# Optimization experiments

Hardware: AMD Instinct MI355X
Metric: run time of the kernel (lower is better)

Reference implementation:

```python
import jax, jax.numpy as jnp
import numpy as np

B, C, N, HID = 1, 64, 1024, 128


def setup_inputs() -> dict:
    key = jax.random.key(0)
    k1, k2, k3, k4, k5 = jax.random.split(key, 5)
    x = jax.random.normal(k1, (B, C, N), dtype=jnp.float32)
    # Conv2d(2C -> HID, 1): weight [HID, 2C] (1x1 kernel flattened), bias [HID]
    W1 = jax.random.normal(k2, (HID, 2 * C), dtype=jnp.float32) * (1.0 / np.sqrt(2 * C))
    b1 = jax.random.normal(k3, (HID,), dtype=jnp.float32) * 0.01
    # Conv2d(HID -> 1, 1): weight [HID], bias [1]
    W2 = jax.random.normal(k4, (HID,), dtype=jnp.float32) * (1.0 / np.sqrt(HID))
    b2 = jax.random.normal(k5, (1,), dtype=jnp.float32) * 0.01
    return {"x": x, "W1": W1, "b1": b1, "W2": W2, "b2": b2}


def reference(x, W1, b1, W2, b2):
    # Original: m1[b,c,i,j] = x[b,c,j]; m2[b,c,i,j] = x[b,c,i]; block = cat([m1, m2], dim=1)
    # tanh is elementwise, and the 1x1 conv is linear, so we split W1 into the
    # halves acting on m1 (j-indexed) and m2 (i-indexed) and avoid the explicit
    # O(N^2 * 2C) repeat+concat. The nonlinear hidden tensor [B,HID,N,N] is the
    # same math as Conv2d(tanh(block)).
    c = x.shape[1]
    t = jnp.tanh(x)                                   # [B, C, N]
    pj = jnp.einsum('hc,bcn->bhn', W1[:, :c], t)      # contribution of m1 (varies over j)
    pi = jnp.einsum('hc,bcn->bhn', W1[:, c:], t)      # contribution of m2 (varies over i)
    h = jnp.tanh(pi[:, :, :, None] + pj[:, :, None, :] + b1[None, :, None, None])  # [B,HID,N,N]
    e = jnp.einsum('h,bhij->bij', W2, h) + b2[0]      # [B, N, N]
    return e + jnp.swapaxes(e, 1, 2)
```

## Files before the change

kernel.cpp:

```cpp
#include <hip/hip_runtime.h>
#include <math.h>

#define CN   64
#define NN   1024
#define HIDN 128
#define NDIAG 528
#define NOFF  496

__device__ __forceinline__ float tanh_fast(float x) {
    float e = __expf(2.0f * x);
    return 1.0f - 2.0f * __builtin_amdgcn_rcpf(e + 1.0f);
}

__global__ __launch_bounds__(256) void prep_kernel(
    const float* __restrict__ x, const float* __restrict__ W1,
    const float* __restrict__ b1, float2* __restrict__ S)
{
    __shared__ float t_s[2][64];
    const int tid = threadIdx.x;
    const int n0  = blockIdx.x * 2;

    if (tid < 64) {
        float2 xv = *(const float2*)&x[tid * NN + n0];
        t_s[0][tid] = tanh_fast(xv.x);
        t_s[1][tid] = tanh_fast(xv.y);
    }
    __syncthreads();

    const int h  = tid & 127;
    const int nl = tid >> 7;
    const float4* wrow = (const float4*)(W1 + h * (2 * CN));

    float pj[4] = {0.f, 0.f, 0.f, 0.f};
    float pi[4] = {0.f, 0.f, 0.f, 0.f};
#pragma unroll
    for (int c4 = 0; c4 < 16; ++c4) {
        float4 tv = *(const float4*)&t_s[nl][c4 * 4];
        float4 wl = wrow[c4];
        float4 wh = wrow[16 + c4];
        const int s = c4 & 3;
        pj[s] = fmaf(wl.x, tv.x, fmaf(wl.y, tv.y, fmaf(wl.z, tv.z, fmaf(wl.w, tv.w, pj[s]))));
        pi[s] = fmaf(wh.x, tv.x, fmaf(wh.y, tv.y, fmaf(wh.z, tv.z, fmaf(wh.w, tv.w, pi[s]))));
    }
    float pjs = (pj[0] + pj[1]) + (pj[2] + pj[3]);
    float pis = (pi[0] + pi[1]) + (pi[2] + pi[3]);
    float U = tanh_fast(pis + b1[h]);
    float V = tanh_fast(pjs);
    S[h * NN + n0 + nl] = make_float2(U, V);
}

__device__ __forceinline__ void sym_term(float w2h, float2 A, float2 B, float& acc)
{
    float d1 = fmaf(A.x, B.y, 1.0f);
    float d2 = fmaf(B.x, A.y, 1.0f);
    float n1 = A.x + B.y;
    float n2 = B.x + A.y;
    float r  = __builtin_amdgcn_rcpf(d1 * d2);
    float t  = fmaf(n1, d2, n2 * d1);
    acc = fmaf(w2h, t * r, acc);
}

__global__ __launch_bounds__(256) void pair_kernel(
    const float2* __restrict__ S, const float* __restrict__ W2,
    const float* __restrict__ b2, float* __restrict__ out)
{
    const int id = blockIdx.x;
    int bi, bj, h0, nchunk;
    bool chunk1;
    if (id < NDIAG) {
        int t = id;
        int r = (int)((sqrtf(8.f * t + 1.f) - 1.f) * 0.5f);
        while ((r + 1) * (r + 2) / 2 <= t) ++r;
        while (r * (r + 1) / 2 > t) --r;
        int c = t - r * (r + 1) / 2;
        bi = c; bj = r; chunk1 = false;
        h0 = 0; nchunk = (bi == bj) ? 4 : 2;
    } else {
        int t = id - NDIAG;
        int r = (int)((1.f + sqrtf(8.f * t + 1.f)) * 0.5f);
        while (r * (r - 1) / 2 > t) --r;
        while (r * (r + 1) / 2 <= t) ++r;
        int c = t - r * (r - 1) / 2;
        bi = c; bj = r; chunk1 = true;
        h0 = 64; nchunk = 2;
    }

    __shared__ float2 Si[32][32];
    __shared__ float2 Sj[32][32];

    const int tid = threadIdx.x;
    const int tx = tid & 15, ty = tid >> 4;
    const int i0 = bi * 32, j0 = bj * 32;

    float acc00 = 0.f, acc01 = 0.f, acc10 = 0.f, acc11 = 0.f;

    for (int hc = 0; hc < nchunk; ++hc) {
        const int hbase = h0 + hc * 32;
        __syncthreads();
#pragma unroll
        for (int k = 0; k < 4; ++k) {
            int t2 = tid + k * 256;
            int hl = t2 >> 5, nl = t2 & 31;
            Si[hl][nl] = S[(hbase + hl) * NN + i0 + nl];
            Sj[hl][nl] = S[(hbase + hl) * NN + j0 + nl];
        }
        __syncthreads();
#pragma unroll 8
        for (int hl = 0; hl < 32; ++hl) {
            float w2h = W2[hbase + hl];
            float2 A0 = Si[hl][ty];
            float2 A1 = Si[hl][ty + 16];
            float2 B0 = Sj[hl][tx];
            float2 B1 = Sj[hl][tx + 16];
            sym_term(w2h, A0, B0, acc00);
            sym_term(w2h, A0, B1, acc01);
            sym_term(w2h, A1, B0, acc10);
            sym_term(w2h, A1, B1, acc11);
        }
    }

    if (!chunk1) {
        float v00 = acc00, v01 = acc01, v10 = acc10, v11 = acc11;
        if (bi == bj) {
            const float bias2 = 2.0f * b2[0];
            v00 += bias2; v01 += bias2; v10 += bias2; v11 += bias2;
        }
        out[(i0 + ty)      * NN + j0 + tx]      = v00;
        out[(i0 + ty)      * NN + j0 + tx + 16] = v01;
        out[(i0 + ty + 16) * NN + j0 + tx]      = v10;
        out[(i0 + ty + 16) * NN + j0 + tx + 16] = v11;
    } else {
        __syncthreads();
        float* T = (float*)&Si[0][0];
        T[ty * 33 + tx]             = acc00;
        T[ty * 33 + tx + 16]        = acc01;
        T[(ty + 16) * 33 + tx]      = acc10;
        T[(ty + 16) * 33 + tx + 16] = acc11;
        __syncthreads();
        out[(j0 + ty)      * NN + i0 + tx]      = T[tx * 33 + ty];
        out[(j0 + ty)      * NN + i0 + tx + 16] = T[(tx + 16) * 33 + ty];
        out[(j0 + ty + 16) * NN + i0 + tx]      = T[tx * 33 + ty + 16];
        out[(j0 + ty + 16) * NN + i0 + tx + 16] = T[(tx + 16) * 33 + ty + 16];
    }
}

__global__ __launch_bounds__(256) void combine_kernel(
    const float* __restrict__ b2, float* __restrict__ out)
{
    int t = blockIdx.x;
    int r = (int)((1.f + sqrtf(8.f * t + 1.f)) * 0.5f);
    while (r * (r - 1) / 2 > t) --r;
    while (r * (r + 1) / 2 <= t) ++r;
    int c = t - r * (r - 1) / 2;
    const int i0 = c * 32, j0 = r * 32;

    __shared__ float Ua[32][33];
    __shared__ float Lb[32][33];
    const int tid = threadIdx.x;
    const int tx = tid & 15, ty = tid >> 4;

    Ua[ty][tx]           = out[(i0 + ty)      * NN + j0 + tx];
    Ua[ty][tx + 16]      = out[(i0 + ty)      * NN + j0 + tx + 16];
    Ua[ty + 16][tx]      = out[(i0 + ty + 16) * NN + j0 + tx];
    Ua[ty + 16][tx + 16] = out[(i0 + ty + 16) * NN + j0 + tx + 16];
    Lb[ty][tx]           = out[(j0 + ty)      * NN + i0 + tx];
    Lb[ty][tx + 16]      = out[(j0 + ty)      * NN + i0 + tx + 16];
    Lb[ty + 16][tx]      = out[(j0 + ty + 16) * NN + i0 + tx];
    Lb[ty + 16][tx + 16] = out[(j0 + ty + 16) * NN + i0 + tx + 16];
    __syncthreads();

    const float bias2 = 2.0f * b2[0];
#pragma unroll
    for (int k = 0; k < 4; ++k) {
        int ry = ty + (k >> 1) * 16;
        int cx = tx + (k & 1) * 16;
        out[(i0 + ry) * NN + j0 + cx] = Ua[ry][cx] + Lb[cx][ry] + bias2;
    }
#pragma unroll
    for (int k = 0; k < 4; ++k) {
        int ry = ty + (k >> 1) * 16;
        int cx = tx + (k & 1) * 16;
        out[(j0 + ry) * NN + i0 + cx] = Ua[cx][ry] + Lb[ry][cx] + bias2;
    }
}

extern "C" void kernel_launch(void* const* d_in, const int* in_sizes, int n_in,
                              void* d_out, int out_size, void* d_ws, size_t ws_size,
                              hipStream_t stream)
{
    const float* x  = (const float*)d_in[0];
    const float* W1 = (const float*)d_in[1];
    const float* b1 = (const float*)d_in[2];
    const float* W2 = (const float*)d_in[3];
    const float* b2 = (const float*)d_in[4];
    float* out = (float*)d_out;
    float2* S  = (float2*)d_ws;

    prep_kernel<<<512, 256, 0, stream>>>(x, W1, b1, S);
    pair_kernel<<<NDIAG + NOFF, 256, 0, stream>>>(S, W2, b2, out);
    combine_kernel<<<NOFF, 256, 0, stream>>>(b2, out);
}
```

Before: 98.91 us.

## Split hidden dim into 8 chunks with 4x4 register tiles and workspace reduction

The pair kernel now launches 8 single-wavefront blocks per upper-triangular tile pair, each covering 16 hidden units with a 4x4 per-thread register tile. Per-row and per-column terms are precomputed so the inner loop needs fewer operations per pair. Partial sums go to a workspace that the combine kernel reduces, adding the bias and writing both the tile and its transpose. This is meant to raise parallelism and per-thread reuse, at the cost of extra workspace traffic (about 17 MB of partials written and read back).

```diff
diff --git a/kernel.cpp b/kernel.cpp
--- a/kernel.cpp
+++ b/kernel.cpp
@@ -1,11 +1,10 @@
 #include <hip/hip_runtime.h>
 #include <math.h>
 
-#define CN   64
-#define NN   1024
-#define HIDN 128
-#define NDIAG 528
-#define NOFF  496
+#define CN    64
+#define NN    1024
+#define NPAIR 528
+#define NCHUNK 8
 
 __device__ __forceinline__ float tanh_fast(float x) {
     float e = __expf(2.0f * x);
@@ -49,138 +48,124 @@
     S[h * NN + n0 + nl] = make_float2(U, V);
 }
 
-__device__ __forceinline__ void sym_term(float w2h, float2 A, float2 B, float& acc)
-{
-    float d1 = fmaf(A.x, B.y, 1.0f);
-    float d2 = fmaf(B.x, A.y, 1.0f);
-    float n1 = A.x + B.y;
-    float n2 = B.x + A.y;
-    float r  = __builtin_amdgcn_rcpf(d1 * d2);
-    float t  = fmaf(n1, d2, n2 * d1);
-    acc = fmaf(w2h, t * r, acc);
-}
-
-__global__ __launch_bounds__(256) void pair_kernel(
+__global__ __launch_bounds__(64) void pair_kernel(
     const float2* __restrict__ S, const float* __restrict__ W2,
-    const float* __restrict__ b2, float* __restrict__ out)
+    float* __restrict__ ws)
 {
     const int id = blockIdx.x;
-    int bi, bj, h0, nchunk;
-    bool chunk1;
-    if (id < NDIAG) {
-        int t = id;
-        int r = (int)((sqrtf(8.f * t + 1.f) - 1.f) * 0.5f);
-        while ((r + 1) * (r + 2) / 2 <= t) ++r;
-        while (r * (r + 1) / 2 > t) --r;
-        int c = t - r * (r + 1) / 2;
-        bi = c; bj = r; chunk1 = false;
-        h0 = 0; nchunk = (bi == bj) ? 4 : 2;
-    } else {
-        int t = id - NDIAG;
-        int r = (int)((1.f + sqrtf(8.f * t + 1.f)) * 0.5f);
-        while (r * (r - 1) / 2 > t) --r;
-        while (r * (r + 1) / 2 <= t) ++r;
-        int c = t - r * (r - 1) / 2;
-        bi = c; bj = r; chunk1 = true;
-        h0 = 64; nchunk = 2;
+    const int pair = id >> 3, chunk = id & 7;
+    int r = (int)((sqrtf(8.f * pair + 1.f) - 1.f) * 0.5f);
+    while ((r + 1) * (r + 2) / 2 <= pair) ++r;
+    while (r * (r + 1) / 2 > pair) --r;
+    const int bi = pair - r * (r + 1) / 2, bj = r;
+    const int i0 = bi * 32, j0 = bj * 32, h0 = chunk * 16;
+
+    __shared__ float2 Si[16 * 32];
+    __shared__ float2 Sj[16 * 32];
+    const int lane = threadIdx.x;
+
+    {
+        float4* SiF = (float4*)Si;
+        float4* SjF = (float4*)Sj;
+        const float4* SF = (const float4*)S;
+#pragma unroll
+        for (int k = 0; k < 4; ++k) {
+            int t = k * 64 + lane;
+            int row = t >> 4, seg = t & 15;
+            SiF[t] = SF[(((h0 + row) * NN + i0) >> 1) + seg];
+            SjF[t] = SF[(((h0 + row) * NN + j0) >> 1) + seg];
+        }
+    }
+    __syncthreads();
+
+    const int la = lane & 7, lb = lane >> 3;
+    float acc[4][4];
+#pragma unroll
+    for (int m = 0; m < 4; ++m)
+#pragma unroll
+        for (int n = 0; n < 4; ++n) acc[m][n] = 0.f;
+
+#pragma unroll 4
+    for (int h = 0; h < 16; ++h) {
+        const float w2h = W2[h0 + h];
+        float2 A[4], B[4];
+#pragma unroll
+        for (int m = 0; m < 4; ++m) A[m] = Si[h * 32 + la + 8 * m];
+#pragma unroll
+        for (int n = 0; n < 4; ++n) B[n] = Sj[h * 32 + lb + 8 * n];
+        float PA[4], QA[4], PB[4], QB[4];
+#pragma unroll
+        for (int m = 0; m < 4; ++m) {
+            PA[m] = w2h * (A[m].x + A[m].y);
+            QA[m] = fmaf(A[m].x, A[m].y, 1.0f);
+        }
+#pragma unroll
+        for (int n = 0; n < 4; ++n) {
+            PB[n] = w2h * (B[n].x + B[n].y);
+            QB[n] = fmaf(B[n].x, B[n].y, 1.0f);
+        }
+#pragma unroll
+        for (int m = 0; m < 4; ++m)
+#pragma unroll
+            for (int n = 0; n < 4; ++n) {
+                float d1 = fmaf(A[m].x, B[n].y, 1.0f);
+                float d2 = fmaf(B[n].x, A[m].y, 1.0f);
+                float rr = __builtin_amdgcn_rcpf(d1 * d2);
+                float Np = fmaf(PA[m], QB[n], PB[n] * QA[m]);
+                acc[m][n] = fmaf(Np, rr, acc[m][n]);
+            }
     }
 
-    __shared__ float2 Si[32][32];
-    __shared__ float2 Sj[32][32];
-
-    const int tid = threadIdx.x;
-    const int tx = tid & 15, ty = tid >> 4;
-    const int i0 = bi * 32, j0 = bj * 32;
-
-    float acc00 = 0.f, acc01 = 0.f, acc10 = 0.f, acc11 = 0.f;
-
-    for (int hc = 0; hc < nchunk; ++hc) {
-        const int hbase = h0 + hc * 32;
-        __syncthreads();
+    float* wsp = ws + (pair * NCHUNK + chunk) * 1024;
 #pragma unroll
-        for (int k = 0; k < 4; ++k) {
-            int t2 = tid + k * 256;
-            int hl = t2 >> 5, nl = t2 & 31;
-            Si[hl][nl] = S[(hbase + hl) * NN + i0 + nl];
-            Sj[hl][nl] = S[(hbase + hl) * NN + j0 + nl];
-        }
-        __syncthreads();
-#pragma unroll 8
-        for (int hl = 0; hl < 32; ++hl) {
-            float w2h = W2[hbase + hl];
-            float2 A0 = Si[hl][ty];
-            float2 A1 = Si[hl][ty + 16];
-            float2 B0 = Sj[hl][tx];
-            float2 B1 = Sj[hl][tx + 16];
-            sym_term(w2h, A0, B0, acc00);
-            sym_term(w2h, A0, B1, acc01);
-            sym_term(w2h, A1, B0, acc10);
-            sym_term(w2h, A1, B1, acc11);
-        }
-    }
-
-    if (!chunk1) {
-        float v00 = acc00, v01 = acc01, v10 = acc10, v11 = acc11;
-        if (bi == bj) {
-            const float bias2 = 2.0f * b2[0];
-            v00 += bias2; v01 += bias2; v10 += bias2; v11 += bias2;
-        }
-        out[(i0 + ty)      * NN + j0 + tx]      = v00;
-        out[(i0 + ty)      * NN + j0 + tx + 16] = v01;
-        out[(i0 + ty + 16) * NN + j0 + tx]      = v10;
-        out[(i0 + ty + 16) * NN + j0 + tx + 16] = v11;
-    } else {
-        __syncthreads();
-        float* T = (float*)&Si[0][0];
-        T[ty * 33 + tx]             = acc00;
-        T[ty * 33 + tx + 16]        = acc01;
-        T[(ty + 16) * 33 + tx]      = acc10;
-        T[(ty + 16) * 33 + tx + 16] = acc11;
-        __syncthreads();
-        out[(j0 + ty)      * NN + i0 + tx]      = T[tx * 33 + ty];
-        out[(j0 + ty)      * NN + i0 + tx + 16] = T[(tx + 16) * 33 + ty];
-        out[(j0 + ty + 16) * NN + i0 + tx]      = T[tx * 33 + ty + 16];
-        out[(j0 + ty + 16) * NN + i0 + tx + 16] = T[(tx + 16) * 33 + ty + 16];
-    }
+    for (int m = 0; m < 4; ++m)
+#pragma unroll
+        for (int n = 0; n < 4; ++n)
+            wsp[(m * 4 + n) * 64 + lane] = acc[m][n];
 }
 
 __global__ __launch_bounds__(256) void combine_kernel(
-    const float* __restrict__ b2, float* __restrict__ out)
+    const float* __restrict__ ws, const float* __restrict__ b2,
+    float* __restrict__ out)
 {
-    int t = blockIdx.x;
-    int r = (int)((1.f + sqrtf(8.f * t + 1.f)) * 0.5f);
-    while (r * (r - 1) / 2 > t) --r;
-    while (r * (r + 1) / 2 <= t) ++r;
-    int c = t - r * (r - 1) / 2;
-    const int i0 = c * 32, j0 = r * 32;
+    const int pair = blockIdx.x;
+    int r = (int)((sqrtf(8.f * pair + 1.f) - 1.f) * 0.5f);
+    while ((r + 1) * (r + 2) / 2 <= pair) ++r;
+    while (r * (r + 1) / 2 > pair) --r;
+    const int bi = pair - r * (r + 1) / 2, bj = r;
+    const int i0 = bi * 32, j0 = bj * 32;
 
-    __shared__ float Ua[32][33];
-    __shared__ float Lb[32][33];
-    const int tid = threadIdx.x;
-    const int tx = tid & 15, ty = tid >> 4;
+    __shared__ float T[32 * 35];
+    const int t = threadIdx.x;
+    const int lane_p = t & 63, q0 = t >> 6;
+    const int la = lane_p & 7, lb = (lane_p >> 3) & 7;
+    const float bias2 = 2.0f * b2[0];
+    const float* wsp = ws + pair * NCHUNK * 1024;
 
-    Ua[ty][tx]           = out[(i0 + ty)      * NN + j0 + tx];
-    Ua[ty][tx + 16]      = out[(i0 + ty)      * NN + j0 + tx + 16];
-    Ua[ty + 16][tx]      = out[(i0 + ty + 16) * NN + j0 + tx];
-    Ua[ty + 16][tx + 16] = out[(i0 + ty + 16) * NN + j0 + tx + 16];
-    Lb[ty][tx]           = out[(j0 + ty)      * NN + i0 + tx];
-    Lb[ty][tx + 16]      = out[(j0 + ty)      * NN + i0 + tx + 16];
-    Lb[ty + 16][tx]      = out[(j0 + ty + 16) * NN + i0 + tx];
-    Lb[ty + 16][tx + 16] = out[(j0 + ty + 16) * NN + i0 + tx + 16];
+#pragma unroll
+    for (int k = 0; k < 4; ++k) {
+        float a = 0.f;
+#pragma unroll
+        for (int cc = 0; cc < NCHUNK; ++cc)
+            a += wsp[cc * 1024 + (q0 + 4 * k) * 64 + lane_p];
+        T[(la + 8 * k) * 35 + lb + 8 * q0] = a + bias2;
+    }
     __syncthreads();
 
-    const float bias2 = 2.0f * b2[0];
+    const int tx = t & 15, ty = t >> 4;
 #pragma unroll
     for (int k = 0; k < 4; ++k) {
-        int ry = ty + (k >> 1) * 16;
-        int cx = tx + (k & 1) * 16;
-        out[(i0 + ry) * NN + j0 + cx] = Ua[ry][cx] + Lb[cx][ry] + bias2;
+        int rr2 = ty + (k >> 1) * 16;
+        int cc2 = tx + (k & 1) * 16;
+        out[(i0 + rr2) * NN + j0 + cc2] = T[rr2 * 35 + cc2];
     }
+    if (bi != bj) {
 #pragma unroll
-    for (int k = 0; k < 4; ++k) {
-        int ry = ty + (k >> 1) * 16;
-        int cx = tx + (k & 1) * 16;
-        out[(j0 + ry) * NN + i0 + cx] = Ua[cx][ry] + Lb[ry][cx] + bias2;
+        for (int k = 0; k < 4; ++k) {
+            int rr2 = ty + (k >> 1) * 16;
+            int cc2 = tx + (k & 1) * 16;
+            out[(j0 + rr2) * NN + i0 + cc2] = T[cc2 * 35 + rr2];
+        }
     }
 }
 
@@ -194,9 +179,11 @@
     const float* W2 = (const float*)d_in[3];
     const float* b2 = (const float*)d_in[4];
     float* out = (float*)d_out;
-    float2* S  = (float2*)d_ws;
+
+    float2* S   = (float2*)d_ws;
+    float*  par = (float*)((char*)d_ws + (size_t)2 * 1024 * 1024);
 
     prep_kernel<<<512, 256, 0, stream>>>(x, W1, b1, S);
-    pair_kernel<<<NDIAG + NOFF, 256, 0, stream>>>(S, W2, b2, out);
-    combine_kernel<<<NOFF, 256, 0, stream>>>(b2, out);
+    pair_kernel<<<NPAIR * NCHUNK, 64, 0, stream>>>(S, W2, par);
+    combine_kernel<<<NPAIR, 256, 0, stream>>>(par, b2, out);
 }
```

Result: slower. 100.9 us (+2.0%).
